# Kernel optimization log

Measured on AMD Instinct MI355X. Metric: run time of the kernel, lower is better.

Reference implementation:

```python
import jax, jax.numpy as jnp
import numpy as np

B, S, T, D, H, FF = 2, 512, 64, 256, 8, 1024
DK = D // H
EPS = 1e-5


def setup_inputs() -> dict:
    key = jax.random.key(0)
    ks = jax.random.split(key, 24)
    sc = 1.0 / np.sqrt(D)
    inp = {"x": jax.random.normal(ks[0], (B, S, T, D), jnp.float32)}
    names = ["tq", "tk", "tv", "to", "sq", "sk", "sv", "so"]
    for i, n in enumerate(names):
        inp[n + "_w"] = jax.random.normal(ks[1 + 2 * i], (D, D), jnp.float32) * sc
        inp[n + "_b"] = jax.random.normal(ks[2 + 2 * i], (D,), jnp.float32) * sc
    inp["fc1_w"] = jax.random.normal(ks[17], (D, FF), jnp.float32) * sc
    inp["fc1_b"] = jnp.zeros((FF,), jnp.float32)
    inp["fc2_w"] = jax.random.normal(ks[18], (FF, D), jnp.float32) * (1.0 / np.sqrt(FF))
    inp["fc2_b"] = jnp.zeros((D,), jnp.float32)
    inp["ln1_w"] = jnp.ones((D,), jnp.float32)
    inp["ln1_b"] = jnp.zeros((D,), jnp.float32)
    inp["ln2_w"] = jnp.ones((D,), jnp.float32)
    inp["ln2_b"] = jnp.zeros((D,), jnp.float32)
    return inp


def _heads(x, w, b):
    # (B,S,T,D) -> (B,H,S,T,DK)
    Bx, Sx, Tx, Dx = x.shape
    return (x @ w + b).reshape(Bx, Sx, Tx, H, Dx // H).transpose(0, 3, 1, 2, 4)


def _merge(o, w, b):
    # (B,H,S,T,DK) -> (B,S,T,D)
    Bx, Hx, Sx, Tx, dk = o.shape
    return o.transpose(0, 2, 3, 1, 4).reshape(Bx, Sx, Tx, Hx * dk) @ w + b


def _ln(x, g, b):
    m = jnp.mean(x, -1, keepdims=True)
    v = jnp.mean((x - m) ** 2, -1, keepdims=True)
    return (x - m) * jax.lax.rsqrt(v + EPS) * g + b


def _forward(x, tq_w, tq_b, tk_w, tk_b, tv_w, tv_b, to_w, to_b,
             sq_w, sq_b, sk_w, sk_b, sv_w, sv_b, so_w, so_b,
             fc1_w, fc1_b, fc2_w, fc2_b, ln1_w, ln1_b, ln2_w, ln2_b):
    scale = 1.0 / np.sqrt(DK)
    # --- time attention (over T, independent per space point s) ---
    q = _heads(x, tq_w, tq_b)
    k = _heads(x, tk_w, tk_b)
    v = _heads(x, tv_w, tv_b)
    p = jax.nn.softmax(jnp.einsum('bhstd,bhsud->bhstu', q, k) * scale, axis=-1)
    tt = _merge(jnp.einsum('bhstu,bhsud->bhstd', p, v), to_w, to_b)
    # --- space attention (over S, independent per time step t) ---
    q = _heads(tt, sq_w, sq_b)
    k = _heads(tt, sk_w, sk_b)
    v = _heads(tt, sv_w, sv_b)
    p = jax.nn.softmax(jnp.einsum('bhstd,bhutd->bhtsu', q, k) * scale, axis=-1)
    so = _merge(jnp.einsum('bhtsu,bhutd->bhstd', p, v), so_w, so_b)
    # --- residual + post-LN, then FFN + residual + post-LN ---
    h = _ln(x + so, ln1_w, ln1_b)
    ff = jax.nn.relu(h @ fc1_w + fc1_b) @ fc2_w + fc2_b
    return _ln(h + ff, ln2_w, ln2_b)


def reference(x, tq_w, tq_b, tk_w, tk_b, tv_w, tv_b, to_w, to_b,
              sq_w, sq_b, sk_w, sk_b, sv_w, sv_b, so_w, so_b,
              fc1_w, fc1_b, fc2_w, fc2_b, ln1_w, ln1_b, ln2_w, ln2_b):
    return _forward(x, tq_w, tq_b, tk_w, tk_b, tv_w, tv_b, to_w, to_b,
                    sq_w, sq_b, sk_w, sk_b, sv_w, sv_b, so_w, so_b,
                    fc1_w, fc1_b, fc2_w, fc2_b, ln1_w, ln1_b, ln2_w, ln2_b)
```

## Files before the change

### kernel.cpp

```cpp
#include <hip/hip_runtime.h>
#include <hip/hip_bf16.h>

#define BB   2
#define SS   512
#define TT_  64
#define DD   256
#define HH   8
#define DKK  32
#define FFF  1024
#define NTOK 65536
#define EPSV 1e-5f
#define SCALE 0.17677669529663687f
#define S2F   0.25503486f
#define KPS  40
#define KP   40
#define VH   136
#define VP6  80

typedef unsigned short u16;
typedef unsigned int   u32;
typedef __attribute__((ext_vector_type(8))) short bf16x8;
typedef __attribute__((ext_vector_type(4))) short bf16x4;
typedef __attribute__((ext_vector_type(4))) float f32x4;

#if __has_builtin(__builtin_amdgcn_exp2f)
#define EXP2(x) __builtin_amdgcn_exp2f(x)
#else
#define EXP2(x) exp2f(x)
#endif

__device__ __forceinline__ float bf2f(u32 u) {
    union { u32 i; float f; } c; c.i = u << 16; return c.f;
}
__device__ __forceinline__ u16 f2bf(float f) {
    __hip_bfloat16 h = __float2bfloat16(f);
    return *reinterpret_cast<u16*>(&h);
}
__device__ __forceinline__ u32 cvtpk2(float lo, float hi) {
    float2 f; f.x = lo; f.y = hi;
    __hip_bfloat162 h2 = __float22bfloat162_rn(f);
    union { __hip_bfloat162 h; u32 u; } c; c.h = h2;
    return c.u;
}
__device__ __forceinline__ void load8v(const float* p, float* v) {
    *(float4*)(v)     = *(const float4*)(p);
    *(float4*)(v + 4) = *(const float4*)(p + 4);
}
__device__ __forceinline__ void load8v(const u16* p, float* v) {
    uint4 raw = *(const uint4*)(p);
    v[0] = bf2f(raw.x & 0xffffu); v[1] = bf2f(raw.x >> 16);
    v[2] = bf2f(raw.y & 0xffffu); v[3] = bf2f(raw.y >> 16);
    v[4] = bf2f(raw.z & 0xffffu); v[5] = bf2f(raw.z >> 16);
    v[6] = bf2f(raw.w & 0xffffu); v[7] = bf2f(raw.w >> 16);
}
__device__ __forceinline__ void load4v(const float* p, float* v) {
    float4 t = *(const float4*)p; v[0] = t.x; v[1] = t.y; v[2] = t.z; v[3] = t.w;
}
__device__ __forceinline__ void load4v(const u16* p, float* v) {
    uint2 raw = *(const uint2*)p;
    v[0] = bf2f(raw.x & 0xffffu); v[1] = bf2f(raw.x >> 16);
    v[2] = bf2f(raw.y & 0xffffu); v[3] = bf2f(raw.y >> 16);
}
__device__ __forceinline__ uint4 pack8bf(const float* v) {
    uint4 r;
    r.x = cvtpk2(v[0], v[1]); r.y = cvtpk2(v[2], v[3]);
    r.z = cvtpk2(v[4], v[5]); r.w = cvtpk2(v[6], v[7]);
    return r;
}
__device__ __forceinline__ uint2 pack4bf(const float* v) {
    uint2 r;
    r.x = cvtpk2(v[0], v[1]); r.y = cvtpk2(v[2], v[3]);
    return r;
}
__device__ __forceinline__ bf16x4 packbf4(const float* v) {
    union { uint2 u; bf16x4 h; } c;
    c.u = pack4bf(v);
    return c.h;
}
__device__ __forceinline__ void store4o(float* p, const float* v) {
    float4 t; t.x = v[0]; t.y = v[1]; t.z = v[2]; t.w = v[3];
    *(float4*)p = t;
}
__device__ __forceinline__ void store4o(u16* p, const float* v) {
    *(uint2*)p = pack4bf(v);
}
__device__ __forceinline__ float rload(const float* p) { return *p; }
__device__ __forceinline__ float rload(const u16* p)  { return bf2f(*p); }
__device__ __forceinline__ void sstore(float* p, float v) { *p = v; }
__device__ __forceinline__ void sstore(u16* p, float v)   { *p = f2bf(v); }
__device__ __forceinline__ void gl16(const u16* gsrc, u16* ldst) {
    __builtin_amdgcn_global_load_lds(
        (const __attribute__((address_space(1))) void*)gsrc,
        (__attribute__((address_space(3))) void*)ldst, 16, 0, 0);
}

#if __has_builtin(__builtin_amdgcn_mfma_f32_16x16x16bf16_1k)
__device__ __forceinline__ f32x4 mfma16(bf16x4 a, bf16x4 b, f32x4 c) {
    return __builtin_amdgcn_mfma_f32_16x16x16bf16_1k(a, b, c, 0, 0, 0);
}
#else
__device__ __forceinline__ f32x4 mfma16(bf16x4 a, bf16x4 b, f32x4 c) {
    asm("v_mfma_f32_16x16x16_bf16 %0, %1, %2, %0" : "+v"(c) : "v"(a), "v"(b));
    return c;
}
#endif

#define BF16_ONE ((short)0x3F80)

__global__ __launch_bounds__(256)
void transpose_w(const float* __restrict__ W, u16* __restrict__ WT, int K, int M,
                 float scale)
{
    __shared__ float t[32][33];
    const int mb = blockIdx.x * 32;
    const int kb = blockIdx.y * 32;
    const int lx = threadIdx.x & 31;
    const int ly = threadIdx.x >> 5;
    #pragma unroll
    for (int i = ly; i < 32; i += 8) t[i][lx] = W[(size_t)(kb + i) * M + mb + lx];
    __syncthreads();
    #pragma unroll
    for (int i = ly; i < 32; i += 8) WT[(size_t)(mb + i) * K + kb + lx] = f2bf(t[lx][i] * scale);
}

__global__ __launch_bounds__(256)
void transpose_w4(const float* __restrict__ W0, const float* __restrict__ W1,
                  const float* __restrict__ W2, const float* __restrict__ W3,
                  u16* __restrict__ T0, u16* __restrict__ T1,
                  u16* __restrict__ T2, u16* __restrict__ T3, float s0)
{
    __shared__ float t[32][33];
    const int z = blockIdx.z;
    const float* W = (z == 0) ? W0 : (z == 1) ? W1 : (z == 2) ? W2 : W3;
    u16*       WT = (z == 0) ? T0 : (z == 1) ? T1 : (z == 2) ? T2 : T3;
    const float scale = (z == 0) ? s0 : 1.0f;
    const int mb = blockIdx.x * 32;
    const int kb = blockIdx.y * 32;
    const int lx = threadIdx.x & 31;
    const int ly = threadIdx.x >> 5;
    #pragma unroll
    for (int i = ly; i < 32; i += 8) t[i][lx] = W[(size_t)(kb + i) * DD + mb + lx];
    __syncthreads();
    #pragma unroll
    for (int i = ly; i < 32; i += 8) WT[(size_t)(mb + i) * DD + kb + lx] = f2bf(t[lx][i] * scale);
}

__global__ __launch_bounds__(256)
void pack_bias3(const float* __restrict__ a, const float* __restrict__ b,
                const float* __restrict__ c, float* __restrict__ out, float s0)
{
    const int i = threadIdx.x;
    out[i] = a[i] * s0; out[256 + i] = b[i]; out[512 + i] = c[i];
}

__global__ __launch_bounds__(256)
void fuse_to_sqkv_w(const float* __restrict__ to_w,
                    const float* __restrict__ sq_w, const float* __restrict__ sk_w,
                    const float* __restrict__ sv_w, u16* __restrict__ wt_out)
{
    const int m = blockIdx.x;
    const int k = threadIdx.x;
    const float* Wsq = (m < 256) ? sq_w : (m < 512 ? sk_w : sv_w);
    const int mc = m & 255;
    float acc = 0.f;
    for (int j = 0; j < 256; j++)
        acc += to_w[k * 256 + j] * Wsq[j * 256 + mc];
    if (m < 256) acc *= S2F;
    wt_out[m * 256 + k] = f2bf(acc);
}
__global__ __launch_bounds__(256)
void fuse_to_sqkv_b(const float* __restrict__ to_b,
                    const float* __restrict__ sq_w, const float* __restrict__ sk_w,
                    const float* __restrict__ sv_w,
                    const float* __restrict__ sq_b, const float* __restrict__ sk_b,
                    const float* __restrict__ sv_b, float* __restrict__ b_out)
{
    const int m = blockIdx.x * 256 + threadIdx.x;
    const float* Wsq = (blockIdx.x == 0) ? sq_w : (blockIdx.x == 1 ? sk_w : sv_w);
    const float* bs  = (blockIdx.x == 0) ? sq_b : (blockIdx.x == 1 ? sk_b : sv_b);
    const int mc = m & 255;
    float acc = bs[mc];
    for (int j = 0; j < 256; j++) acc += to_b[j] * Wsq[j * 256 + mc];
    if (blockIdx.x == 0) acc *= S2F;
    b_out[m] = acc;
}

__global__ __launch_bounds__(256)
void cvt_bf16(const float* __restrict__ in, u16* __restrict__ out, int n8)
{
    for (int i = blockIdx.x * blockDim.x + threadIdx.x; i < n8; i += gridDim.x * blockDim.x) {
        float v[8];
        load8v(in + (size_t)i * 8, v);
        *(uint4*)(out + (size_t)i * 8) = pack8bf(v);
    }
}

__global__ __launch_bounds__(512)
void gemm_bt7(const u16* __restrict__ A, int lda,
              const u16* __restrict__ WT,
              const float* __restrict__ bias, u16* __restrict__ C,
              int K, int M, int relu)
{
    __shared__ u16 As0a[256 * 32];
    __shared__ u16 As0b[256 * 32];
    __shared__ u16 As1a[256 * 32];
    __shared__ u16 As1b[256 * 32];
    __shared__ u16 Bs0a[256 * 32];
    __shared__ u16 Bs0b[256 * 32];
    __shared__ u16 Bs1a[256 * 32];
    __shared__ u16 Bs1b[256 * 32];
    const int tid  = threadIdx.x;
    const int wid  = tid >> 6;
    const int lane = tid & 63;
    const int l16  = lane & 15;
    const int kg   = lane >> 4;

    const int gx  = gridDim.x;
    const int nwg = gridDim.x * gridDim.y;
    int lin = blockIdx.y * gridDim.x + blockIdx.x;
    lin = (lin & 7) * (nwg >> 3) + (lin >> 3);
    const int row0 = (lin / gx) * 256;
    const int col0 = (lin % gx) * 256;

    const int srow = lane >> 2;
    const int gchunk = ((lane & 3) ^ ((srow >> 1) & 3)) * 8;
    const int rchunk = (kg ^ ((l16 >> 1) & 3)) * 8;

    const u16* Abase = A  + (size_t)(row0 + wid * 32 + srow) * lda + gchunk;
    const u16* Bbase = WT + (size_t)(col0 + wid * 32 + srow) * K + gchunk;

    f32x4 acc[2][16];
    #pragma unroll
    for (int fr = 0; fr < 2; fr++)
        #pragma unroll
        for (int fc = 0; fc < 16; fc++)
            acc[fr][fc] = (f32x4){0.f, 0.f, 0.f, 0.f};

#define STAGE_B7(ASA, ASB2, BSA, BSB2, k0)                                      \
    do {                                                                        \
        _Pragma("unroll")                                                       \
        for (int q = 0; q < 2; q++) {                                           \
            const int rbase = wid * 32 + q * 16;                                \
            gl16(Abase + (size_t)(q * 16) * lda + (k0),      &ASA[rbase * 32]); \
            gl16(Abase + (size_t)(q * 16) * lda + (k0) + 32, &ASB2[rbase * 32]);\
            gl16(Bbase + (size_t)(q * 16) * K   + (k0),      &BSA[rbase * 32]); \
            gl16(Bbase + (size_t)(q * 16) * K   + (k0) + 32, &BSB2[rbase * 32]);\
        }                                                                       \
    } while (0)

#define COMPUTE_B7(ASB, BSB)                                                    \
    do {                                                                        \
        bf16x8 af[2];                                                           \
        _Pragma("unroll")                                                       \
        for (int fr = 0; fr < 2; fr++)                                          \
            af[fr] = *(const bf16x8*)(&ASB[(wid * 32 + fr * 16 + l16) * 32 + rchunk]); \
        _Pragma("unroll")                                                       \
        for (int fc = 0; fc < 16; fc++) {                                       \
            bf16x8 bfr = *(const bf16x8*)(&BSB[(fc * 16 + l16) * 32 + rchunk]); \
            acc[0][fc] = __builtin_amdgcn_mfma_f32_16x16x32_bf16(af[0], bfr, acc[0][fc], 0, 0, 0); \
            acc[1][fc] = __builtin_amdgcn_mfma_f32_16x16x32_bf16(af[1], bfr, acc[1][fc], 0, 0, 0); \
        }                                                                       \
    } while (0)

    STAGE_B7(As0a, As0b, Bs0a, Bs0b, 0);
    __syncthreads();

    for (int k0 = 0; k0 < K; k0 += 128) {
        if (k0 + 64 < K) STAGE_B7(As1a, As1b, Bs1a, Bs1b, k0 + 64);
        COMPUTE_B7(As0a, Bs0a);
        COMPUTE_B7(As0b, Bs0b);
        __syncthreads();
        if (k0 + 128 < K) STAGE_B7(As0a, As0b, Bs0a, Bs0b, k0 + 128);
        COMPUTE_B7(As1a, Bs1a);
        COMPUTE_B7(As1b, Bs1b);
        __syncthreads();
    }
#undef STAGE_B7
#undef COMPUTE_B7

    #pragma unroll
    for (int fr = 0; fr < 2; fr++) {
        #pragma unroll
        for (int fc = 0; fc < 16; fc++) {
            const int col = col0 + fc * 16 + l16;
            const float bv = bias[col];
            const int row = row0 + wid * 32 + fr * 16 + kg * 4;
            #pragma unroll
            for (int j = 0; j < 4; j += 2) {
                float x0 = acc[fr][fc][j]     + bv;
                float x1 = acc[fr][fc][j + 1] + bv;
                if (relu) { x0 = fmaxf(x0, 0.f); x1 = fmaxf(x1, 0.f); }
                const u32 pk = cvtpk2(x0, x1);
                C[(size_t)(row + j)     * M + col] = (u16)pk;
                C[(size_t)(row + j + 1) * M + col] = (u16)(pk >> 16);
            }
        }
    }
}

__global__ __launch_bounds__(512)
void gemm_bt6(const u16* __restrict__ A, int lda,
              const u16* __restrict__ WT,
              const float* __restrict__ bias, u16* __restrict__ C,
              int K, int M, int relu)
{
    __shared__ u16 As0[256 * 32];
    __shared__ u16 As1[256 * 32];
    __shared__ u16 Bs0[128 * 32];
    __shared__ u16 Bs1[128 * 32];
    const int tid  = threadIdx.x;
    const int wid  = tid >> 6;
    const int lane = tid & 63;
    const int l16  = lane & 15;
    const int kg   = lane >> 4;

    const int nwg = gridDim.x * gridDim.y;
    int lin = blockIdx.y * gridDim.x + blockIdx.x;
    lin = (lin & 7) * (nwg >> 3) + (lin >> 3);
    const int row0 = (lin / gridDim.x) * 256;
    const int col0 = (lin % gridDim.x) * 128;

    const int srow = lane >> 2;
    const int gchunk = ((lane & 3) ^ ((srow >> 1) & 3)) * 8;
    const int rchunk = (kg ^ ((l16 >> 1) & 3)) * 8;

    const u16* Abase = A  + (size_t)(row0 + srow) * lda + gchunk;
    const u16* Bbase = WT + (size_t)(col0 + wid * 16 + srow) * K + gchunk;

    f32x4 acc[2][8];
    #pragma unroll
    for (int fr = 0; fr < 2; fr++)
        #pragma unroll
        for (int fc = 0; fc < 8; fc++)
            acc[fr][fc] = (f32x4){0.f, 0.f, 0.f, 0.f};

#define STAGE_T(ASB, BSB, k0)                                                   \
    do {                                                                        \
        _Pragma("unroll")                                                       \
        for (int q = 0; q < 2; q++) {                                           \
            const int rbase = wid * 32 + q * 16;                                \
            gl16(Abase + (size_t)rbase * lda + (k0), &ASB[rbase * 32]);         \
        }                                                                       \
        gl16(Bbase + (k0), &BSB[wid * 16 * 32]);                                \
    } while (0)

#define COMPUTE_T(ASB, BSB)                                                     \
    do {                                                                        \
        bf16x8 af[2], bfr[8];                                                   \
        _Pragma("unroll")                                                       \
        for (int fr = 0; fr < 2; fr++)                                          \
            af[fr] = *(const bf16x8*)(&ASB[(wid * 32 + fr * 16 + l16) * 32 + rchunk]); \
        _Pragma("unroll")                                                       \
        for (int fc = 0; fc < 8; fc++)                                          \
            bfr[fc] = *(const bf16x8*)(&BSB[(fc * 16 + l16) * 32 + rchunk]);    \
        _Pragma("unroll")                                                       \
        for (int fr = 0; fr < 2; fr++)                                          \
            _Pragma("unroll")                                                   \
            for (int fc = 0; fc < 8; fc++)                                      \
                acc[fr][fc] = __builtin_amdgcn_mfma_f32_16x16x32_bf16(af[fr], bfr[fc], acc[fr][fc], 0, 0, 0); \
    } while (0)

    STAGE_T(As0, Bs0, 0);
    __syncthreads();

    for (int k0 = 0; k0 < K; k0 += 64) {
        if (k0 + 32 < K) STAGE_T(As1, Bs1, k0 + 32);
        COMPUTE_T(As0, Bs0);
        __syncthreads();
        if (k0 + 64 < K) STAGE_T(As0, Bs0, k0 + 64);
        COMPUTE_T(As1, Bs1);
        __syncthreads();
    }
#undef STAGE_T
#undef COMPUTE_T

    #pragma unroll
    for (int fr = 0; fr < 2; fr++) {
        #pragma unroll
        for (int fc = 0; fc < 8; fc++) {
            const int col = col0 + fc * 16 + l16;
            const float bv = bias[col];
            const int row = row0 + wid * 32 + fr * 16 + kg * 4;
            #pragma unroll
            for (int j = 0; j < 4; j += 2) {
                float x0 = acc[fr][fc][j]     + bv;
                float x1 = acc[fr][fc][j + 1] + bv;
                if (relu) { x0 = fmaxf(x0, 0.f); x1 = fmaxf(x1, 0.f); }
                const u32 pk = cvtpk2(x0, x1);
                C[(size_t)(row + j)     * M + col] = (u16)pk;
                C[(size_t)(row + j + 1) * M + col] = (u16)(pk >> 16);
            }
        }
    }
}

__global__ __launch_bounds__(512)
void gemm_bt6h(const u16* __restrict__ A, int lda,
               const u16* __restrict__ WT,
               const float* __restrict__ bias, u16* __restrict__ C,
               int K, int M, int relu)
{
    __shared__ u16 As0[128 * 32];
    __shared__ u16 As1[128 * 32];
    __shared__ u16 Bs0[128 * 32];
    __shared__ u16 Bs1[128 * 32];
    const int tid  = threadIdx.x;
    const int wid  = tid >> 6;
    const int lane = tid & 63;
    const int l16  = lane & 15;
    const int kg   = lane >> 4;

    const int nwg = gridDim.x * gridDim.y;
    int lin = blockIdx.y * gridDim.x + blockIdx.x;
    lin = (lin & 7) * (nwg >> 3) + (lin >> 3);
    const int row0 = (lin / gridDim.x) * 128;
    const int col0 = (lin % gridDim.x) * 128;

    const int srow = lane >> 2;
    const int gchunk = ((lane & 3) ^ ((srow >> 1) & 3)) * 8;
    const int rchunk = (kg ^ ((l16 >> 1) & 3)) * 8;

    const u16* Abase = A  + (size_t)(row0 + wid * 16 + srow) * lda + gchunk;
    const u16* Bbase = WT + (size_t)(col0 + wid * 16 + srow) * K + gchunk;

    f32x4 acc[8];
    #pragma unroll
    for (int fc = 0; fc < 8; fc++)
        acc[fc] = (f32x4){0.f, 0.f, 0.f, 0.f};

#define STAGE_H(ASB, BSB, k0)                                                   \
    do {                                                                        \
        gl16(Abase + (k0), &ASB[wid * 16 * 32]);                                \
        gl16(Bbase + (k0), &BSB[wid * 16 * 32]);                                \
    } while (0)

#define COMPUTE_H(ASB, BSB)                                                     \
    do {                                                                        \
        bf16x8 af, bfr[8];                                                      \
        af = *(const bf16x8*)(&ASB[(wid * 16 + l16) * 32 + rchunk]);            \
        _Pragma("unroll")                                                       \
        for (int fc = 0; fc < 8; fc++)                                          \
            bfr[fc] = *(const bf16x8*)(&BSB[(fc * 16 + l16) * 32 + rchunk]);    \
        _Pragma("unroll")                                                       \
        for (int fc = 0; fc < 8; fc++)                                          \
            acc[fc] = __builtin_amdgcn_mfma_f32_16x16x32_bf16(af, bfr[fc], acc[fc], 0, 0, 0); \
    } while (0)

    STAGE_H(As0, Bs0, 0);
    __syncthreads();

    for (int k0 = 0; k0 < K; k0 += 64) {
        if (k0 + 32 < K) STAGE_H(As1, Bs1, k0 + 32);
        COMPUTE_H(As0, Bs0);
        __syncthreads();
        if (k0 + 64 < K) STAGE_H(As0, Bs0, k0 + 64);
        COMPUTE_H(As1, Bs1);
        __syncthreads();
    }
#undef STAGE_H
#undef COMPUTE_H

    #pragma unroll
    for (int fc = 0; fc < 8; fc++) {
        const int col = col0 + fc * 16 + l16;
        const float bv = bias[col];
        const int row = row0 + wid * 16 + kg * 4;
        #pragma unroll
        for (int j = 0; j < 4; j += 2) {
            float x0 = acc[fc][j]     + bv;
            float x1 = acc[fc][j + 1] + bv;
            if (relu) { x0 = fmaxf(x0, 0.f); x1 = fmaxf(x1, 0.f); }
            const u32 pk = cvtpk2(x0, x1);
            C[(size_t)(row + j)     * M + col] = (u16)pk;
            C[(size_t)(row + j + 1) * M + col] = (u16)(pk >> 16);
        }
    }
}

template<typename TR, typename TO>
__global__ __launch_bounds__(512)
void gemm_ln2(const u16* __restrict__ A, int lda,
              const u16* __restrict__ WT,
              const float* __restrict__ bias,
              const TR* __restrict__ R,
              const float* __restrict__ gw, const float* __restrict__ bw,
              TO* __restrict__ out, int K)
{
    __shared__ u16 As0a[256 * 32];
    __shared__ u16 As0b[256 * 32];
    __shared__ u16 As1a[256 * 32];
    __shared__ u16 As1b[256 * 32];
    __shared__ u16 Bs0a[256 * 32];
    __shared__ u16 Bs0b[256 * 32];
    __shared__ u16 Bs1a[256 * 32];
    __shared__ u16 Bs1b[256 * 32];
    const int tid  = threadIdx.x;
    const int wid  = tid >> 6;
    const int lane = tid & 63;
    const int l16  = lane & 15;
    const int kg   = lane >> 4;

    const int nwg = gridDim.x;
    int lin = blockIdx.x;
    lin = (lin & 7) * (nwg >> 3) + (lin >> 3);
    const int row0 = lin * 256;

    const int srow = lane >> 2;
    const int gchunk = ((lane & 3) ^ ((srow >> 1) & 3)) * 8;
    const int rchunk = (kg ^ ((l16 >> 1) & 3)) * 8;

    const u16* Abase = A  + (size_t)(row0 + wid * 32 + srow) * lda + gchunk;
    const u16* Bbase = WT + (size_t)(wid * 32 + srow) * K + gchunk;

    f32x4 acc[2][16];
    #pragma unroll
    for (int fr = 0; fr < 2; fr++)
        #pragma unroll
        for (int fc = 0; fc < 16; fc++)
            acc[fr][fc] = (f32x4){0.f, 0.f, 0.f, 0.f};

#define STAGE_L2(ASA, ASB2, BSA, BSB2, k0)                                      \
    do {                                                                        \
        _Pragma("unroll")                                                       \
        for (int q = 0; q < 2; q++) {                                           \
            const int rbase = wid * 32 + q * 16;                                \
            gl16(Abase + (size_t)(q * 16) * lda + (k0),      &ASA[rbase * 32]); \
            gl16(Abase + (size_t)(q * 16) * lda + (k0) + 32, &ASB2[rbase * 32]);\
            gl16(Bbase + (size_t)(q * 16) * K   + (k0),      &BSA[rbase * 32]); \
            gl16(Bbase + (size_t)(q * 16) * K   + (k0) + 32, &BSB2[rbase * 32]);\
        }                                                                       \
    } while (0)

#define COMPUTE_L2(ASB, BSB)                                                    \
    do {                                                                        \
        bf16x8 af[2];                                                           \
        _Pragma("unroll")                                                       \
        for (int fr = 0; fr < 2; fr++)                                          \
            af[fr] = *(const bf16x8*)(&ASB[(wid * 32 + fr * 16 + l16) * 32 + rchunk]); \
        _Pragma("unroll")                                                       \
        for (int fc = 0; fc < 16; fc++) {                                       \
            bf16x8 bfr = *(const bf16x8*)(&BSB[(fc * 16 + l16) * 32 + rchunk]); \
            acc[0][fc] = __builtin_amdgcn_mfma_f32_16x16x32_bf16(af[0], bfr, acc[0][fc], 0, 0, 0); \
            acc[1][fc] = __builtin_amdgcn_mfma_f32_16x16x32_bf16(af[1], bfr, acc[1][fc], 0, 0, 0); \
        }                                                                       \
    } while (0)

    STAGE_L2(As0a, As0b, Bs0a, Bs0b, 0);
    __syncthreads();

    for (int k0 = 0; k0 < K; k0 += 128) {
        if (k0 + 64 < K) STAGE_L2(As1a, As1b, Bs1a, Bs1b, k0 + 64);
        COMPUTE_L2(As0a, Bs0a);
        COMPUTE_L2(As0b, Bs0b);
        __syncthreads();
        if (k0 + 128 < K) STAGE_L2(As0a, As0b, Bs0a, Bs0b, k0 + 128);
        COMPUTE_L2(As1a, Bs1a);
        COMPUTE_L2(As1b, Bs1b);
        __syncthreads();
    }
#undef STAGE_L2
#undef COMPUTE_L2

    float bia[16], gwv[16], bwv[16];
    #pragma unroll
    for (int fc = 0; fc < 16; fc++) {
        const int d = fc * 16 + l16;
        bia[fc] = bias[d]; gwv[fc] = gw[d]; bwv[fc] = bw[d];
    }
    #pragma unroll
    for (int fr = 0; fr < 2; fr++) {
        #pragma unroll
        for (int j = 0; j < 4; j++) {
            const int row = row0 + wid * 32 + fr * 16 + kg * 4 + j;
            const size_t rb = (size_t)row * DD + l16;
            float v[16];
            float s1 = 0.f, s2 = 0.f;
            #pragma unroll
            for (int fc = 0; fc < 16; fc++) {
                const float xv = acc[fr][fc][j] + bia[fc] + rload(R + rb + fc * 16);
                v[fc] = xv; s1 += xv; s2 += xv * xv;
            }
            #pragma unroll
            for (int o = 1; o < 16; o <<= 1) { s1 += __shfl_xor(s1, o); s2 += __shfl_xor(s2, o); }
            const float mean = s1 * (1.f / DD);
            const float var  = s2 * (1.f / DD) - mean * mean;
            const float rs   = rsqrtf(var + EPSV);
            #pragma unroll
            for (int fc = 0; fc < 16; fc++)
                sstore(out + rb + fc * 16, (v[fc] - mean) * rs * gwv[fc] + bwv[fc]);
        }
    }
}

__global__ __launch_bounds__(256)
void time_attn12(const u16* __restrict__ F, int ld, u16* __restrict__ O)
{
    __shared__ u16 Ks2[2][64 * KP];
    __shared__ u16 Vt2[2][32 * VP6];
    const int bid = blockIdx.x;
    const int tid  = threadIdx.x;
    const int wid  = tid >> 6;
    const int lane = tid & 63;
    const int l16  = lane & 15;
    const int g    = lane >> 4;

    #pragma unroll
    for (int it = 0; it < 2; it++) {
        const int i = tid + it * 256;
        const int tu = i >> 8, rr = (i >> 2) & 63, p = i & 3;
        const int tau = bid * 2 + tu;
        const size_t ga = ((size_t)(tau >> 3) * 64 + rr) * ld + (tau & 7) * DKK + 256 + p * 8;
        *(uint4*)&Ks2[tu][rr * KP + p * 8] = *(const uint4*)(F + ga);
    }
    #pragma unroll
    for (int it = 0; it < 2; it++) {
        const int i = tid + it * 256;
        const int tu = i >> 8, p = (i >> 6) & 3, rr = i & 63;
        const int tau = bid * 2 + tu;
        const size_t ga = ((size_t)(tau >> 3) * 64 + rr) * ld + (tau & 7) * DKK + 512 + p * 8;
        uint4 vv = *(const uint4*)(F + ga);
        const u16* vp = (const u16*)&vv;
        #pragma unroll
        for (int j = 0; j < 8; j++) Vt2[tu][(p * 8 + j) * VP6 + rr] = vp[j];
    }
    __syncthreads();

    const int tu  = wid >> 1;
    const int tau = bid * 2 + tu;
    const int hc  = (tau & 7) * DKK;
    const size_t n0 = (size_t)(tau >> 3) * 64;
    const int q0  = (wid & 1) * 32;
    const f32x4 z4 = (f32x4){0.f, 0.f, 0.f, 0.f};
    const bf16x4 vone = (bf16x4){BF16_ONE, BF16_ONE, BF16_ONE, BF16_ONE};

    bf16x8 qf[2];
    #pragma unroll
    for (int f = 0; f < 2; f++)
        qf[f] = *(const bf16x8*)(F + (n0 + q0 + f * 16 + l16) * ld + hc + g * 8);

    f32x4 s[2][4];
    #pragma unroll
    for (int kt = 0; kt < 4; kt++) {
        bf16x8 kf = *(const bf16x8*)&Ks2[tu][(kt * 16 + l16) * KP + g * 8];
        s[0][kt] = __builtin_amdgcn_mfma_f32_16x16x32_bf16(kf, qf[0], z4, 0, 0, 0);
        s[1][kt] = __builtin_amdgcn_mfma_f32_16x16x32_bf16(kf, qf[1], z4, 0, 0, 0);
    }

    bf16x4 pp[2][4];
    #pragma unroll
    for (int f = 0; f < 2; f++) {
        #pragma unroll
        for (int kt = 0; kt < 4; kt++) {
            float pv[4];
            #pragma unroll
            for (int j = 0; j < 4; j++) pv[j] = EXP2(s[f][kt][j]);
            pp[f][kt] = packbf4(pv);
        }
    }

    f32x4 o[2][2];
    f32x4 lacc[2];
    #pragma unroll
    for (int f = 0; f < 2; f++) {
        lacc[f] = z4;
        #pragma unroll
        for (int hh = 0; hh < 2; hh++)
            o[f][hh] = z4;
    }
    #pragma unroll
    for (int kt = 0; kt < 4; kt++) {
        bf16x4 vf[2];
        #pragma unroll
        for (int hh = 0; hh < 2; hh++)
            vf[hh] = *(const bf16x4*)&Vt2[tu][(hh * 16 + l16) * VP6 + kt * 16 + g * 4];
        #pragma unroll
        for (int f = 0; f < 2; f++) {
            o[f][0] = mfma16(pp[f][kt], vf[0], o[f][0]);
            o[f][1] = mfma16(pp[f][kt], vf[1], o[f][1]);
            lacc[f] = mfma16(pp[f][kt], vone, lacc[f]);
        }
    }

    #pragma unroll
    for (int f = 0; f < 2; f++) {
        float iv[4];
        #pragma unroll
        for (int j = 0; j < 4; j++) iv[j] = 1.f / lacc[f][j];
        #pragma unroll
        for (int hh = 0; hh < 2; hh++) {
            const u32 p0 = cvtpk2(o[f][hh][0] * iv[0], o[f][hh][1] * iv[1]);
            const u32 p1 = cvtpk2(o[f][hh][2] * iv[2], o[f][hh][3] * iv[3]);
            const size_t ga0 = (n0 + q0 + f * 16 + g * 4) * DD + hc + hh * 16 + l16;
            O[ga0]          = (u16)p0;
            O[ga0 + DD]     = (u16)(p0 >> 16);
            O[ga0 + 2 * DD] = (u16)p1;
            O[ga0 + 3 * DD] = (u16)(p1 >> 16);
        }
    }
}

__global__ __launch_bounds__(512, 4)
void space_attn16(u16* __restrict__ F, int ld)
{
    __shared__ u16 Ks[2][128 * KPS];
    __shared__ u16 Vt[2][32 * VH];
    const int bid = blockIdx.x;
    const int t  = bid & (TT_ - 1);
    const int h  = (bid >> 6) & (HH - 1);
    const int b  = bid >> 9;
    const int hc = h * DKK;
    const int tid  = threadIdx.x;
    const int wid  = tid >> 6;
    const int lane = tid & 63;
    const int l16  = lane & 15;
    const int g    = lane >> 4;

    const int kr = tid >> 2, kp = tid & 3;
    const int vr = tid & 127, vp = tid >> 7;
    const size_t rowstr = (size_t)TT_ * ld;
    const size_t base0  = ((size_t)(b * SS) * TT_ + t) * ld + hc;

    const int q0 = wid * 64;
    bf16x8 qf[4];
    #pragma unroll
    for (int f = 0; f < 4; f++) {
        const int s = q0 + f * 16 + l16;
        qf[f] = *(const bf16x8*)(F + base0 + (size_t)s * rowstr + g * 8);
    }

    uint4 kreg = *(const uint4*)(F + base0 + 256 + (size_t)kr * rowstr + kp * 8);
    uint4 vreg = *(const uint4*)(F + base0 + 512 + (size_t)vr * rowstr + vp * 8);
    *(uint4*)&Ks[0][kr * KPS + kp * 8] = kreg;
    {
        const u16* vpp = (const u16*)&vreg;
        #pragma unroll
        for (int j = 0; j < 8; j++) Vt[0][(vp * 8 + j) * VH + vr] = vpp[j];
    }
    __syncthreads();

    f32x4 o[4][2];
    f32x4 lacc[4];
    const f32x4 z4 = (f32x4){0.f, 0.f, 0.f, 0.f};
    const bf16x4 vone = (bf16x4){BF16_ONE, BF16_ONE, BF16_ONE, BF16_ONE};
    #pragma unroll
    for (int f = 0; f < 4; f++) {
        lacc[f] = z4;
        #pragma unroll
        for (int hh = 0; hh < 2; hh++)
            o[f][hh] = z4;
    }

    for (int qtr = 0; qtr < 4; qtr++) {
        const int cur = qtr & 1;
        if (qtr < 3) {
            const int key = (qtr + 1) * 128;
            kreg = *(const uint4*)(F + base0 + 256 + (size_t)(key + kr) * rowstr + kp * 8);
            vreg = *(const uint4*)(F + base0 + 512 + (size_t)(key + vr) * rowstr + vp * 8);
        }

        for (int kc2 = 0; kc2 < 4; kc2++) {
            bf16x8 kfa = *(const bf16x8*)&Ks[cur][(kc2 * 32 +      l16) * KPS + g * 8];
            bf16x8 kfb = *(const bf16x8*)&Ks[cur][(kc2 * 32 + 16 + l16) * KPS + g * 8];

            bf16x4 pa[4], pb[4];
            #pragma unroll
            for (int f = 0; f < 4; f++) {
                f32x4 sa = __builtin_amdgcn_mfma_f32_16x16x32_bf16(kfa, qf[f], z4, 0, 0, 0);
                f32x4 sb = __builtin_amdgcn_mfma_f32_16x16x32_bf16(kfb, qf[f], z4, 0, 0, 0);
                float pva[4], pvb[4];
                #pragma unroll
                for (int j = 0; j < 4; j++) pva[j] = EXP2(sa[j]);
                #pragma unroll
                for (int j = 0; j < 4; j++) pvb[j] = EXP2(sb[j]);
                pa[f] = packbf4(pva);
                pb[f] = packbf4(pvb);
            }

            bf16x4 va[2][2];
            #pragma unroll
            for (int hh = 0; hh < 2; hh++)
                #pragma unroll
                for (int u = 0; u < 2; u++)
                    va[hh][u] = *(const bf16x4*)&Vt[cur][(hh * 16 + l16) * VH + kc2 * 32 + u * 16 + g * 4];

            __builtin_amdgcn_s_setprio(1);
            #pragma unroll
            for (int f = 0; f < 4; f++) {
                #pragma unroll
                for (int hh = 0; hh < 2; hh++) {
                    o[f][hh] = mfma16(pa[f], va[hh][0], o[f][hh]);
                    o[f][hh] = mfma16(pb[f], va[hh][1], o[f][hh]);
                }
                lacc[f] = mfma16(pa[f], vone, lacc[f]);
                lacc[f] = mfma16(pb[f], vone, lacc[f]);
            }
            __builtin_amdgcn_s_setprio(0);
        }

        if (qtr < 3) {
            __syncthreads();
            *(uint4*)&Ks[cur ^ 1][kr * KPS + kp * 8] = kreg;
            const u16* vpp = (const u16*)&vreg;
            #pragma unroll
            for (int j = 0; j < 8; j++) Vt[cur ^ 1][(vp * 8 + j) * VH + vr] = vpp[j];
            __syncthreads();
        }
    }

    #pragma unroll
    for (int f = 0; f < 4; f++) {
        float iv[4];
        #pragma unroll
        for (int j = 0; j < 4; j++) iv[j] = 1.f / lacc[f][j];
        const int s = q0 + f * 16 + g * 4;
        #pragma unroll
        for (int hh = 0; hh < 2; hh++) {
            const u32 p0 = cvtpk2(o[f][hh][0] * iv[0], o[f][hh][1] * iv[1]);
            const u32 p1 = cvtpk2(o[f][hh][2] * iv[2], o[f][hh][3] * iv[3]);
            const size_t ga0 = base0 + (size_t)s * rowstr + hh * 16 + l16;
            F[ga0]              = (u16)p0;
            F[ga0 + rowstr]     = (u16)(p0 >> 16);
            F[ga0 + 2 * rowstr] = (u16)p1;
            F[ga0 + 3 * rowstr] = (u16)(p1 >> 16);
        }
    }
}

template<typename T1, typename TO>
__global__ __launch_bounds__(256)
void add_ln(const T1* __restrict__ X1, const u16* __restrict__ X2,
            const float* __restrict__ gw, const float* __restrict__ bw,
            TO* __restrict__ out)
{
    const int row  = blockIdx.x * 4 + (threadIdx.x >> 6);
    const int lane = threadIdx.x & 63;
    const size_t base = (size_t)row * DD + lane * 4;
    float v[4], w2[4];
    load4v(X1 + base, v);
    load4v(X2 + base, w2);
    v[0] += w2[0]; v[1] += w2[1]; v[2] += w2[2]; v[3] += w2[3];
    float s1 = v[0] + v[1] + v[2] + v[3];
    float s2 = v[0]*v[0] + v[1]*v[1] + v[2]*v[2] + v[3]*v[3];
    #pragma unroll
    for (int o = 1; o < 64; o <<= 1) { s1 += __shfl_xor(s1, o); s2 += __shfl_xor(s2, o); }
    const float mean = s1 * (1.f / DD);
    const float var  = s2 * (1.f / DD) - mean * mean;
    const float rs   = rsqrtf(var + EPSV);
    float o4[4];
    #pragma unroll
    for (int i = 0; i < 4; i++) {
        const int d = lane * 4 + i;
        o4[i] = (v[i] - mean) * rs * gw[d] + bw[d];
    }
    store4o(out + base, o4);
}

extern "C" void kernel_launch(void* const* d_in, const int* in_sizes, int n_in,
                              void* d_out, int out_size, void* d_ws, size_t ws_size,
                              hipStream_t stream)
{
    (void)in_sizes; (void)n_in; (void)out_size;
    const float* x     = (const float*)d_in[0];
    const float* tq_w  = (const float*)d_in[1];
    const float* tq_b  = (const float*)d_in[2];
    const float* tk_w  = (const float*)d_in[3];
    const float* tk_b  = (const float*)d_in[4];
    const float* tv_w  = (const float*)d_in[5];
    const float* tv_b  = (const float*)d_in[6];
    const float* to_w  = (const float*)d_in[7];
    const float* to_b  = (const float*)d_in[8];
    const float* sq_w  = (const float*)d_in[9];
    const float* sq_b  = (const float*)d_in[10];
    const float* sk_w  = (const float*)d_in[11];
    const float* sk_b  = (const float*)d_in[12];
    const float* sv_w  = (const float*)d_in[13];
    const float* sv_b  = (const float*)d_in[14];
    const float* so_w  = (const float*)d_in[15];
    const float* so_b  = (const float*)d_in[16];
    const float* fc1_w = (const float*)d_in[17];
    const float* fc1_b = (const float*)d_in[18];
    const float* fc2_w = (const float*)d_in[19];
    const float* fc2_b = (const float*)d_in[20];
    const float* ln1_w = (const float*)d_in[21];
    const float* ln1_b = (const float*)d_in[22];
    const float* ln2_w = (const float*)d_in[23];
    const float* ln2_b = (const float*)d_in[24];

    const size_t SLOT = (size_t)NTOK * DD;
    u16*   F  = (u16*)d_ws;
    u16*   OA = (u16*)d_out;
    float* HD = (float*)d_out;

    const bool ffn1 = ws_size >= 6 * SLOT * sizeof(u16);
    u16*   WTb = ffn1 ? ((u16*)d_ws + 4 * SLOT)
                      : (u16*)((char*)d_out + (61u << 20));
    float* BIb = ffn1 ? (float*)((u16*)d_ws + 4 * SLOT + 983040)
                      : (float*)((char*)d_out + (63u << 20));

    u16* wt_tqkv  = WTb;
    u16* wt_fused = wt_tqkv + 3 * 65536;
    u16* wt_so    = wt_fused + 3 * 65536;
    u16* wt_fc1   = wt_so + 65536;
    u16* wt_fc2   = wt_fc1 + 262144;
    float* b_tqkv  = BIb;
    float* b_fused = BIb + 768;

    dim3 blk(256);
    dim3 blk5(512);

    transpose_w4<<<dim3(DD / 32, DD / 32, 4), blk, 0, stream>>>(
        tq_w, tk_w, tv_w, so_w,
        wt_tqkv, wt_tqkv + 65536, wt_tqkv + 2 * 65536, wt_so, S2F);
    transpose_w<<<dim3(FFF / 32, DD / 32), blk, 0, stream>>>(fc1_w, wt_fc1, DD, FFF, 1.0f);
    transpose_w<<<dim3(DD / 32, FFF / 32), blk, 0, stream>>>(fc2_w, wt_fc2, FFF, DD, 1.0f);
    pack_bias3<<<1, blk, 0, stream>>>(tq_b, tk_b, tv_b, b_tqkv, S2F);
    fuse_to_sqkv_w<<<768, blk, 0, stream>>>(to_w, sq_w, sk_w, sv_w, wt_fused);
    fuse_to_sqkv_b<<<3, blk, 0, stream>>>(to_b, sq_w, sk_w, sv_w, sq_b, sk_b, sv_b, b_fused);

    cvt_bf16<<<2048, blk, 0, stream>>>(x, OA, (int)(SLOT / 8));

    dim3 gqkv7(768 / 256, NTOK / 256);

    gemm_bt7<<<gqkv7, blk5, 0, stream>>>(OA, DD, wt_tqkv, b_tqkv, F, DD, 768, 0);
    time_attn12<<<BB * HH * SS / 2, blk, 0, stream>>>(F, 768, OA);

    gemm_bt7<<<gqkv7, blk5, 0, stream>>>(OA, DD, wt_fused, b_fused, F, DD, 768, 0);
    space_attn16<<<BB * HH * TT_, blk5, 0, stream>>>(F, 768);

    if (ffn1) {
        u16* HB   = (u16*)d_ws + 5 * SLOT;
        u16* W1FF = (u16*)d_ws;
        gemm_ln2<float, u16><<<NTOK / 256, blk5, 0, stream>>>(
            F, 768, wt_so, so_b, x, ln1_w, ln1_b, HB, DD);
        gemm_bt7<<<dim3(FFF / 256, NTOK / 256), blk5, 0, stream>>>(
            HB, DD, wt_fc1, fc1_b, W1FF, DD, FFF, 1);
        gemm_ln2<u16, float><<<NTOK / 256, blk5, 0, stream>>>(
            W1FF, FFF, wt_fc2, fc2_b, HB, ln2_w, ln2_b, HD, FFF);
    } else {
        u16* W0 = (u16*)d_ws;
        u16* W1 = W0 + SLOT;
        u16* W2 = W1 + SLOT;
        dim3 gd(DD / 128, NTOK / 256);
        gemm_bt6<<<gd, blk5, 0, stream>>>(F, 768, wt_so, so_b, OA, DD, DD, 0);
        add_ln<float, u16><<<NTOK / 4, blk, 0, stream>>>(x, OA, ln1_w, ln1_b, W0);
        for (int c = 0; c < 4; c++) {
            const size_t off = (size_t)c * 16384 * DD;
            gemm_bt6<<<dim3(FFF / 128, 16384 / 256), blk5, 0, stream>>>(W0 + off, DD, wt_fc1, fc1_b, W1, DD, FFF, 1);
            gemm_bt6h<<<dim3(DD / 128, 16384 / 128), blk5, 0, stream>>>(W1, FFF, wt_fc2, fc2_b, W2, FFF, DD, 0);
            add_ln<u16, float><<<16384 / 4, blk, 0, stream>>>(W0 + off, W2, ln2_w, ln2_b, HD + off);
        }
    }
}
```

Measured before the change: 390.1 us.

## Fuse fp32-to-bf16 input conversion into QKV GEMM and drop 256x256 GEMM

Measured after the change: 422.5 us. +8.3%, slower.

```diff
diff --git a/kernel.cpp b/kernel.cpp
--- a/kernel.cpp
+++ b/kernel.cpp
@@ -185,119 +185,6 @@
     b_out[m] = acc;
 }
 
-__global__ __launch_bounds__(256)
-void cvt_bf16(const float* __restrict__ in, u16* __restrict__ out, int n8)
-{
-    for (int i = blockIdx.x * blockDim.x + threadIdx.x; i < n8; i += gridDim.x * blockDim.x) {
-        float v[8];
-        load8v(in + (size_t)i * 8, v);
-        *(uint4*)(out + (size_t)i * 8) = pack8bf(v);
-    }
-}
-
-__global__ __launch_bounds__(512)
-void gemm_bt7(const u16* __restrict__ A, int lda,
-              const u16* __restrict__ WT,
-              const float* __restrict__ bias, u16* __restrict__ C,
-              int K, int M, int relu)
-{
-    __shared__ u16 As0a[256 * 32];
-    __shared__ u16 As0b[256 * 32];
-    __shared__ u16 As1a[256 * 32];
-    __shared__ u16 As1b[256 * 32];
-    __shared__ u16 Bs0a[256 * 32];
-    __shared__ u16 Bs0b[256 * 32];
-    __shared__ u16 Bs1a[256 * 32];
-    __shared__ u16 Bs1b[256 * 32];
-    const int tid  = threadIdx.x;
-    const int wid  = tid >> 6;
-    const int lane = tid & 63;
-    const int l16  = lane & 15;
-    const int kg   = lane >> 4;
-
-    const int gx  = gridDim.x;
-    const int nwg = gridDim.x * gridDim.y;
-    int lin = blockIdx.y * gridDim.x + blockIdx.x;
-    lin = (lin & 7) * (nwg >> 3) + (lin >> 3);
-    const int row0 = (lin / gx) * 256;
-    const int col0 = (lin % gx) * 256;
-
-    const int srow = lane >> 2;
-    const int gchunk = ((lane & 3) ^ ((srow >> 1) & 3)) * 8;
-    const int rchunk = (kg ^ ((l16 >> 1) & 3)) * 8;
-
-    const u16* Abase = A  + (size_t)(row0 + wid * 32 + srow) * lda + gchunk;
-    const u16* Bbase = WT + (size_t)(col0 + wid * 32 + srow) * K + gchunk;
-
-    f32x4 acc[2][16];
-    #pragma unroll
-    for (int fr = 0; fr < 2; fr++)
-        #pragma unroll
-        for (int fc = 0; fc < 16; fc++)
-            acc[fr][fc] = (f32x4){0.f, 0.f, 0.f, 0.f};
-
-#define STAGE_B7(ASA, ASB2, BSA, BSB2, k0)                                      \
-    do {                                                                        \
-        _Pragma("unroll")                                                       \
-        for (int q = 0; q < 2; q++) {                                           \
-            const int rbase = wid * 32 + q * 16;                                \
-            gl16(Abase + (size_t)(q * 16) * lda + (k0),      &ASA[rbase * 32]); \
-            gl16(Abase + (size_t)(q * 16) * lda + (k0) + 32, &ASB2[rbase * 32]);\
-            gl16(Bbase + (size_t)(q * 16) * K   + (k0),      &BSA[rbase * 32]); \
-            gl16(Bbase + (size_t)(q * 16) * K   + (k0) + 32, &BSB2[rbase * 32]);\
-        }                                                                       \
-    } while (0)
-
-#define COMPUTE_B7(ASB, BSB)                                                    \
-    do {                                                                        \
-        bf16x8 af[2];                                                           \
-        _Pragma("unroll")                                                       \
-        for (int fr = 0; fr < 2; fr++)                                          \
-            af[fr] = *(const bf16x8*)(&ASB[(wid * 32 + fr * 16 + l16) * 32 + rchunk]); \
-        _Pragma("unroll")                                                       \
-        for (int fc = 0; fc < 16; fc++) {                                       \
-            bf16x8 bfr = *(const bf16x8*)(&BSB[(fc * 16 + l16) * 32 + rchunk]); \
-            acc[0][fc] = __builtin_amdgcn_mfma_f32_16x16x32_bf16(af[0], bfr, acc[0][fc], 0, 0, 0); \
-            acc[1][fc] = __builtin_amdgcn_mfma_f32_16x16x32_bf16(af[1], bfr, acc[1][fc], 0, 0, 0); \
-        }                                                                       \
-    } while (0)
-
-    STAGE_B7(As0a, As0b, Bs0a, Bs0b, 0);
-    __syncthreads();
-
-    for (int k0 = 0; k0 < K; k0 += 128) {
-        if (k0 + 64 < K) STAGE_B7(As1a, As1b, Bs1a, Bs1b, k0 + 64);
-        COMPUTE_B7(As0a, Bs0a);
-        COMPUTE_B7(As0b, Bs0b);
-        __syncthreads();
-        if (k0 + 128 < K) STAGE_B7(As0a, As0b, Bs0a, Bs0b, k0 + 128);
-        COMPUTE_B7(As1a, Bs1a);
-        COMPUTE_B7(As1b, Bs1b);
-        __syncthreads();
-    }
-#undef STAGE_B7
-#undef COMPUTE_B7
-
-    #pragma unroll
-    for (int fr = 0; fr < 2; fr++) {
-        #pragma unroll
-        for (int fc = 0; fc < 16; fc++) {
-            const int col = col0 + fc * 16 + l16;
-            const float bv = bias[col];
-            const int row = row0 + wid * 32 + fr * 16 + kg * 4;
-            #pragma unroll
-            for (int j = 0; j < 4; j += 2) {
-                float x0 = acc[fr][fc][j]     + bv;
-                float x1 = acc[fr][fc][j + 1] + bv;
-                if (relu) { x0 = fmaxf(x0, 0.f); x1 = fmaxf(x1, 0.f); }
-                const u32 pk = cvtpk2(x0, x1);
-                C[(size_t)(row + j)     * M + col] = (u16)pk;
-                C[(size_t)(row + j + 1) * M + col] = (u16)(pk >> 16);
-            }
-        }
-    }
-}
-
 __global__ __launch_bounds__(512)
 void gemm_bt6(const u16* __restrict__ A, int lda,
               const u16* __restrict__ WT,
@@ -372,7 +259,6 @@
         __syncthreads();
     }
 #undef STAGE_T
-#undef COMPUTE_T
 
     #pragma unroll
     for (int fr = 0; fr < 2; fr++) {
@@ -392,16 +278,17 @@
             }
         }
     }
+#undef COMPUTE_T
 }
 
 __global__ __launch_bounds__(512)
-void gemm_bt6h(const u16* __restrict__ A, int lda,
+void gemm_bt6f(const float* __restrict__ A, int lda,
                const u16* __restrict__ WT,
                const float* __restrict__ bias, u16* __restrict__ C,
                int K, int M, int relu)
 {
-    __shared__ u16 As0[128 * 32];
-    __shared__ u16 As1[128 * 32];
+    __shared__ u16 As0[256 * 32];
+    __shared__ u16 As1[256 * 32];
     __shared__ u16 Bs0[128 * 32];
     __shared__ u16 Bs1[128 * 32];
     const int tid  = threadIdx.x;
@@ -413,66 +300,98 @@
     const int nwg = gridDim.x * gridDim.y;
     int lin = blockIdx.y * gridDim.x + blockIdx.x;
     lin = (lin & 7) * (nwg >> 3) + (lin >> 3);
-    const int row0 = (lin / gridDim.x) * 128;
+    const int row0 = (lin / gridDim.x) * 256;
     const int col0 = (lin % gridDim.x) * 128;
 
     const int srow = lane >> 2;
     const int gchunk = ((lane & 3) ^ ((srow >> 1) & 3)) * 8;
     const int rchunk = (kg ^ ((l16 >> 1) & 3)) * 8;
 
-    const u16* Abase = A  + (size_t)(row0 + wid * 16 + srow) * lda + gchunk;
-    const u16* Bbase = WT + (size_t)(col0 + wid * 16 + srow) * K + gchunk;
-
-    f32x4 acc[8];
-    #pragma unroll
-    for (int fc = 0; fc < 8; fc++)
-        acc[fc] = (f32x4){0.f, 0.f, 0.f, 0.f};
-
-#define STAGE_H(ASB, BSB, k0)                                                   \
+    const float* Abase = A + (size_t)(row0 + srow) * lda + gchunk;
+    const u16*   Bbase = WT + (size_t)(col0 + wid * 16 + srow) * K + gchunk;
+
+    f32x4 acc[2][8];
+    #pragma unroll
+    for (int fr = 0; fr < 2; fr++)
+        #pragma unroll
+        for (int fc = 0; fc < 8; fc++)
+            acc[fr][fc] = (f32x4){0.f, 0.f, 0.f, 0.f};
+
+    float ar[2][8];
+
+#define LOADA_F(k0)                                                             \
     do {                                                                        \
-        gl16(Abase + (k0), &ASB[wid * 16 * 32]);                                \
-        gl16(Bbase + (k0), &BSB[wid * 16 * 32]);                                \
+        _Pragma("unroll")                                                       \
+        for (int q = 0; q < 2; q++) {                                           \
+            const float* ga = Abase + (size_t)(wid * 32 + q * 16) * lda + (k0); \
+            *(float4*)&ar[q][0] = *(const float4*)(ga);                         \
+            *(float4*)&ar[q][4] = *(const float4*)(ga + 4);                     \
+        }                                                                       \
     } while (0)
 
-#define COMPUTE_H(ASB, BSB)                                                     \
+#define WRITEA_F(ASB)                                                           \
     do {                                                                        \
-        bf16x8 af, bfr[8];                                                      \
-        af = *(const bf16x8*)(&ASB[(wid * 16 + l16) * 32 + rchunk]);            \
+        _Pragma("unroll")                                                       \
+        for (int q = 0; q < 2; q++) {                                           \
+            const int rbase = wid * 32 + q * 16;                                \
+            *(uint4*)&ASB[rbase * 32 + lane * 8] = pack8bf(ar[q]);              \
+        }                                                                       \
+    } while (0)
+
+#define STAGEB_F(BSB, k0) gl16(Bbase + (k0), &BSB[wid * 16 * 32])
+
+#define COMPUTE_F(ASB, BSB)                                                     \
+    do {                                                                        \
+        bf16x8 af[2], bfr[8];                                                   \
+        _Pragma("unroll")                                                       \
+        for (int fr = 0; fr < 2; fr++)                                          \
+            af[fr] = *(const bf16x8*)(&ASB[(wid * 32 + fr * 16 + l16) * 32 + rchunk]); \
         _Pragma("unroll")                                                       \
         for (int fc = 0; fc < 8; fc++)                                          \
             bfr[fc] = *(const bf16x8*)(&BSB[(fc * 16 + l16) * 32 + rchunk]);    \
         _Pragma("unroll")                                                       \
-        for (int fc = 0; fc < 8; fc++)                                          \
-            acc[fc] = __builtin_amdgcn_mfma_f32_16x16x32_bf16(af, bfr[fc], acc[fc], 0, 0, 0); \
+        for (int fr = 0; fr < 2; fr++)                                          \
+            _Pragma("unroll")                                                   \
+            for (int fc = 0; fc < 8; fc++)                                      \
+                acc[fr][fc] = __builtin_amdgcn_mfma_f32_16x16x32_bf16(af[fr], bfr[fc], acc[fr][fc], 0, 0, 0); \
     } while (0)
 
-    STAGE_H(As0, Bs0, 0);
+    LOADA_F(0);
+    STAGEB_F(Bs0, 0);
+    WRITEA_F(As0);
     __syncthreads();
 
     for (int k0 = 0; k0 < K; k0 += 64) {
-        if (k0 + 32 < K) STAGE_H(As1, Bs1, k0 + 32);
-        COMPUTE_H(As0, Bs0);
+        if (k0 + 32 < K) { LOADA_F(k0 + 32); STAGEB_F(Bs1, k0 + 32); }
+        COMPUTE_F(As0, Bs0);
+        if (k0 + 32 < K) WRITEA_F(As1);
         __syncthreads();
-        if (k0 + 64 < K) STAGE_H(As0, Bs0, k0 + 64);
-        COMPUTE_H(As1, Bs1);
+        if (k0 + 64 < K) { LOADA_F(k0 + 64); STAGEB_F(Bs0, k0 + 64); }
+        COMPUTE_F(As1, Bs1);
+        if (k0 + 64 < K) WRITEA_F(As0);
         __syncthreads();
     }
-#undef STAGE_H
-#undef COMPUTE_H
-
-    #pragma unroll
-    for (int fc = 0; fc < 8; fc++) {
-        const int col = col0 + fc * 16 + l16;
-        const float bv = bias[col];
-        const int row = row0 + wid * 16 + kg * 4;
-        #pragma unroll
-        for (int j = 0; j < 4; j += 2) {
-            float x0 = acc[fc][j]     + bv;
-            float x1 = acc[fc][j + 1] + bv;
-            if (relu) { x0 = fmaxf(x0, 0.f); x1 = fmaxf(x1, 0.f); }
-            const u32 pk = cvtpk2(x0, x1);
-            C[(size_t)(row + j)     * M + col] = (u16)pk;
-            C[(size_t)(row + j + 1) * M + col] = (u16)(pk >> 16);
+#undef LOADA_F
+#undef WRITEA_F
+#undef STAGEB_F
+#undef COMPUTE_F
+
+    #pragma unroll
+    for (int fr = 0; fr < 2; fr++) {
+        #pragma unroll
+        for (int fc = 0; fc < 8; fc++) {
+            const int col = col0 + fc * 16 + l16;
+            const float bv = bias[col];
+            const int row = row0 + wid * 32 + fr * 16 + kg * 4;
+            #pragma unroll
+            for (int j = 0; j < 4; j += 2) {
+                float x0 = acc[fr][fc][j]     + bv;
+                float x1 = acc[fr][fc][j + 1] + bv;
+                if (relu) { x0 = fmaxf(x0, 0.f); x1 = fmaxf(x1, 0.f); }
+                const u32 pk = cvtpk2(x0, x1);
+                C[(size_t)(row + j)     * M + col] = (u16)pk;
+                C[(size_t)(row + j + 1) * M + col] = (u16)(pk >> 16);
+            }
         }
     }
 }
@@ -853,6 +772,89 @@
         o4[i] = (v[i] - mean) * rs * gw[d] + bw[d];
     }
     store4o(out + base, o4);
+}
+
+__global__ __launch_bounds__(512)
+void gemm_bt6h(const u16* __restrict__ A, int lda,
+               const u16* __restrict__ WT,
+               const float* __restrict__ bias, u16* __restrict__ C,
+               int K, int M, int relu)
+{
+    __shared__ u16 As0[128 * 32];
+    __shared__ u16 As1[128 * 32];
+    __shared__ u16 Bs0[128 * 32];
+    __shared__ u16 Bs1[128 * 32];
+    const int tid  = threadIdx.x;
+    const int wid  = tid >> 6;
+    const int lane = tid & 63;
+    const int l16  = lane & 15;
+    const int kg   = lane >> 4;
+
+    const int nwg = gridDim.x * gridDim.y;
+    int lin = blockIdx.y * gridDim.x + blockIdx.x;
+    lin = (lin & 7) * (nwg >> 3) + (lin >> 3);
+    const int row0 = (lin / gridDim.x) * 128;
+    const int col0 = (lin % gridDim.x) * 128;
+
+    const int srow = lane >> 2;
+    const int gchunk = ((lane & 3) ^ ((srow >> 1) & 3)) * 8;
+    const int rchunk = (kg ^ ((l16 >> 1) & 3)) * 8;
+
+    const u16* Abase = A  + (size_t)(row0 + wid * 16 + srow) * lda + gchunk;
+    const u16* Bbase = WT + (size_t)(col0 + wid * 16 + srow) * K + gchunk;
+
+    f32x4 acc[8];
+    #pragma unroll
+    for (int fc = 0; fc < 8; fc++)
+        acc[fc] = (f32x4){0.f, 0.f, 0.f, 0.f};
+
+#define STAGE_H(ASB, BSB, k0)                                                   \
+    do {                                                                        \
+        gl16(Abase + (k0), &ASB[wid * 16 * 32]);                                \
+        gl16(Bbase + (k0), &BSB[wid * 16 * 32]);                                \
+    } while (0)
+
+#define COMPUTE_H(ASB, BSB)                                                     \
+    do {                                                                        \
+        bf16x8 af, bfr[8];                                                      \
+        af = *(const bf16x8*)(&ASB[(wid * 16 + l16) * 32 + rchunk]);            \
+        _Pragma("unroll")                                                       \
+        for (int fc = 0; fc < 8; fc++)                                          \
+            bfr[fc] = *(const bf16x8*)(&BSB[(fc * 16 + l16) * 32 + rchunk]);    \
+        _Pragma("unroll")                                                       \
+        for (int fc = 0; fc < 8; fc++)                                          \
+            acc[fc] = __builtin_amdgcn_mfma_f32_16x16x32_bf16(af, bfr[fc], acc[fc], 0, 0, 0); \
+    } while (0)
+
+    STAGE_H(As0, Bs0, 0);
+    __syncthreads();
+
+    for (int k0 = 0; k0 < K; k0 += 64) {
+        if (k0 + 32 < K) STAGE_H(As1, Bs1, k0 + 32);
+        COMPUTE_H(As0, Bs0);
+        __syncthreads();
+        if (k0 + 64 < K) STAGE_H(As0, Bs0, k0 + 64);
+        COMPUTE_H(As1, Bs1);
+        __syncthreads();
+    }
+#undef STAGE_H
+#undef COMPUTE_H
+
+    #pragma unroll
+    for (int fc = 0; fc < 8; fc++) {
+        const int col = col0 + fc * 16 + l16;
+        const float bv = bias[col];
+        const int row = row0 + wid * 16 + kg * 4;
+        #pragma unroll
+        for (int j = 0; j < 4; j += 2) {
+            float x0 = acc[fc][j]     + bv;
+            float x1 = acc[fc][j + 1] + bv;
+            if (relu) { x0 = fmaxf(x0, 0.f); x1 = fmaxf(x1, 0.f); }
+            const u32 pk = cvtpk2(x0, x1);
+            C[(size_t)(row + j)     * M + col] = (u16)pk;
+            C[(size_t)(row + j + 1) * M + col] = (u16)(pk >> 16);
+        }
+    }
 }
 
 extern "C" void kernel_launch(void* const* d_in, const int* in_sizes, int n_in,
@@ -917,14 +919,12 @@
     fuse_to_sqkv_w<<<768, blk, 0, stream>>>(to_w, sq_w, sk_w, sv_w, wt_fused);
     fuse_to_sqkv_b<<<3, blk, 0, stream>>>(to_b, sq_w, sk_w, sv_w, sq_b, sk_b, sv_b, b_fused);
 
-    cvt_bf16<<<2048, blk, 0, stream>>>(x, OA, (int)(SLOT / 8));
-
-    dim3 gqkv7(768 / 256, NTOK / 256);
-
-    gemm_bt7<<<gqkv7, blk5, 0, stream>>>(OA, DD, wt_tqkv, b_tqkv, F, DD, 768, 0);
+    dim3 gqkv(768 / 128, NTOK / 256);
+
+    gemm_bt6f<<<gqkv, blk5, 0, stream>>>(x, DD, wt_tqkv, b_tqkv, F, DD, 768, 0);
     time_attn12<<<BB * HH * SS / 2, blk, 0, stream>>>(F, 768, OA);
 
-    gemm_bt7<<<gqkv7, blk5, 0, stream>>>(OA, DD, wt_fused, b_fused, F, DD, 768, 0);
+    gemm_bt6<<<gqkv, blk5, 0, stream>>>(OA, DD, wt_fused, b_fused, F, DD, 768, 0);
     space_attn16<<<BB * HH * TT_, blk5, 0, stream>>>(F, 768);
 
     if (ffn1) {
@@ -932,7 +932,7 @@
         u16* W1FF = (u16*)d_ws;
         gemm_ln2<float, u16><<<NTOK / 256, blk5, 0, stream>>>(
             F, 768, wt_so, so_b, x, ln1_w, ln1_b, HB, DD);
-        gemm_bt7<<<dim3(FFF / 256, NTOK / 256), blk5, 0, stream>>>(
+        gemm_bt6<<<dim3(FFF / 128, NTOK / 256), blk5, 0, stream>>>(
             HB, DD, wt_fc1, fc1_b, W1FF, DD, FFF, 1);
         gemm_ln2<u16, float><<<NTOK / 256, blk5, 0, stream>>>(
             W1FF, FFF, wt_fc2, fc2_b, HB, ln2_w, ln2_b, HD, FFF);
```
